# Performance work log

Measured on AMD Instinct MI355X. Metric: run time of the kernel, lower is better.

The kernel has to match this reference:

```python
import jax, jax.numpy as jnp
import numpy as np

HEAD = 16

def setup_inputs() -> dict:
    key = jax.random.key(0)
    ks = jax.random.split(key, 8)
    N, L, CT, C, H, W = 32, 77, 512, 512, 32, 32
    return {
        "feature": jax.random.normal(ks[0], (N, C, H, W), dtype=jnp.float32),
        "token": jax.random.normal(ks[1], (N, L, CT), dtype=jnp.float32),
        "Wv": jax.random.normal(ks[2], (C, CT), dtype=jnp.float32) * 0.02,
        "bv": jax.random.normal(ks[3], (C,), dtype=jnp.float32) * 0.02,
        "Wk": jax.random.normal(ks[4], (C, CT), dtype=jnp.float32) * 0.02,
        "bk": jax.random.normal(ks[5], (C,), dtype=jnp.float32) * 0.02,
        "Wq": jax.random.normal(ks[6], (CT, C), dtype=jnp.float32) * 0.02,
        "bq": jax.random.normal(ks[7], (CT,), dtype=jnp.float32) * 0.02,
    }

def reference(feature, token, Wv, bv, Wk, bk, Wq, bq):
    h = HEAD
    N, L, CT = token.shape
    # Faithful to torch: .view(N, CT, L) is a reshape, NOT a transpose
    tok = token.reshape(N, CT, L)
    # 1x1 conv1d projections: (N, C, L)
    v = jnp.einsum('oc,ncl->nol', Wv, tok) + bv[None, :, None]
    k = jnp.einsum('oc,ncl->nol', Wk, tok) + bk[None, :, None]
    v = v.reshape(N, h, -1, L)  # (N, h, d, L)
    k = k.reshape(N, h, -1, L)  # (N, h, d, L)
    # 1x1 conv2d query projection: C -> CT channels
    q = jnp.einsum('oc,nchw->nohw', Wq, feature) + bq[None, :, None, None]
    _, Cq, H, W = q.shape
    q = q.reshape(N, h, Cq // h, H * W).transpose(0, 1, 3, 2)  # (N, h, HW, d)
    scale = 1.0 / jnp.sqrt(jnp.float32(Cq / h))
    scores = jnp.einsum('nhqd,nhdl->nhql', q, k) * scale  # (N, h, HW, L)
    coef = jax.nn.softmax(scores, axis=3)
    proj = jnp.einsum('nhdl,nhql->nhdq', v, coef)  # (N, h, d, HW)
    out = feature + proj.reshape(N, -1, H, W)
    return (out, token)
```

## Files before the change

kernel.cpp:

```cpp
#include <hip/hip_runtime.h>
#include <hip/hip_bf16.h>

#define N_   32
#define L_   77
#define CT_  512
#define C_   512
#define HW_  1024
#define HEAD_ 16
#define DH_  32
#define NL_  (N_ * L_)
#define NLP_ 2496

typedef __attribute__((ext_vector_type(8))) short bf16x8;
typedef __attribute__((ext_vector_type(4))) short bf16x4;
typedef __attribute__((ext_vector_type(4))) float f32x4;

static __device__ __forceinline__ unsigned short f2bf(float f) {
    unsigned int u = __float_as_uint(f);
    unsigned int r = (u + 0x7fffu + ((u >> 16) & 1u)) >> 16;
    return (unsigned short)r;
}

__global__ __launch_bounds__(256) void prep_kernel(
    const float* __restrict__ token,
    const float* __restrict__ Wk, const float* __restrict__ bk,
    const float* __restrict__ Wv, const float* __restrict__ bv,
    unsigned short* __restrict__ tokT, unsigned short* __restrict__ Wkv,
    float* __restrict__ bkv)
{
    const int blk = blockIdx.x;
    const int t = threadIdx.x;
    if (blk < 256) {
        __shared__ float tile[64][81];
        const int n = blk >> 3, c0 = (blk & 7) * 64;
        const float* src = token + (size_t)n * (CT_ * L_) + (size_t)c0 * L_;
        for (int idx = t; idx < 64 * L_; idx += 256) {
            int cc = idx / L_, l = idx - cc * L_;
            tile[cc][l] = src[idx];
        }
        __syncthreads();
        for (int idx = t; idx < L_ * 16; idx += 256) {
            int l = idx >> 4, cq = (idx & 15) * 4;
            ushort4 h;
            h.x = f2bf(tile[cq + 0][l]);
            h.y = f2bf(tile[cq + 1][l]);
            h.z = f2bf(tile[cq + 2][l]);
            h.w = f2bf(tile[cq + 3][l]);
            *(ushort4*)&tokT[((size_t)(n * L_ + l)) * 512 + c0 + cq] = h;
        }
    } else {
        const int wb = blk - 256;
        const int m0 = wb * 32;
        for (int idx = t; idx < 32 * 128; idx += 256) {
            int mr = idx >> 7, c4 = (idx & 127) * 4;
            int m = m0 + mr;
            const float* src = (m < 512) ? (Wk + (size_t)m * 512 + c4)
                                         : (Wv + (size_t)(m - 512) * 512 + c4);
            float4 f = *(const float4*)src;
            ushort4 h; h.x = f2bf(f.x); h.y = f2bf(f.y); h.z = f2bf(f.z); h.w = f2bf(f.w);
            *(ushort4*)&Wkv[(size_t)m * 512 + c4] = h;
        }
        if (wb == 0) {
            for (int idx = t; idx < 1024; idx += 256)
                bkv[idx] = (idx < 512) ? bk[idx] : bv[idx - 512];
        }
    }
}

__global__ __launch_bounds__(256) void wconv_kernel(
    const float* __restrict__ Wq, unsigned short* __restrict__ Wqbf)
{
    const int m0 = blockIdx.x * 32;
    const int t = threadIdx.x;
    for (int idx = t; idx < 32 * 128; idx += 256) {
        int mr = idx >> 7, c4 = (idx & 127) * 4;
        float4 f = *(const float4*)&Wq[(size_t)(m0 + mr) * 512 + c4];
        ushort4 h; h.x = f2bf(f.x); h.y = f2bf(f.y); h.z = f2bf(f.z); h.w = f2bf(f.w);
        *(ushort4*)&Wqbf[(size_t)(m0 + mr) * 512 + c4] = h;
    }
}

__global__ __launch_bounds__(256) void kvgemm_kernel(
    const unsigned short* __restrict__ tokT,
    const unsigned short* __restrict__ Wkv,
    const float* __restrict__ bkv,
    float* __restrict__ kvbuf)
{
    __shared__ unsigned char Ab[128 * 128];
    __shared__ unsigned char Bb[64 * 128];

    const int blk = blockIdx.x;
    const int mt = blk / 39, nt = blk % 39;
    const int m0 = mt * 128, nl0 = nt * 64;
    const int t = threadIdx.x;
    const int lane = t & 63, w = t >> 6;
    const int wr = w >> 1, wc = w & 1;

    f32x4 acc[4][2];
#pragma unroll
    for (int i = 0; i < 4; ++i)
#pragma unroll
        for (int j = 0; j < 2; ++j) acc[i][j] = (f32x4){0.f, 0.f, 0.f, 0.f};

    for (int c0 = 0; c0 < 512; c0 += 64) {
        __syncthreads();
#pragma unroll
        for (int s = 0; s < 4; ++s) {
            int idx = t + s * 256;
            int row = idx >> 3, k8 = idx & 7;
            bf16x8 v = *(const bf16x8*)&Wkv[(size_t)(m0 + row) * 512 + c0 + k8 * 8];
            *(bf16x8*)(Ab + row * 128 + ((k8 * 16) ^ ((row & 7) << 4))) = v;
        }
#pragma unroll
        for (int s = 0; s < 2; ++s) {
            int idx = t + s * 256;
            int row = idx >> 3, k8 = idx & 7;
            bf16x8 v = *(const bf16x8*)&tokT[(size_t)(nl0 + row) * 512 + c0 + k8 * 8];
            *(bf16x8*)(Bb + row * 128 + ((k8 * 16) ^ ((row & 7) << 4))) = v;
        }
        __syncthreads();

#pragma unroll
        for (int ks = 0; ks < 2; ++ks) {
            const int kb = ks * 64 + (lane >> 4) * 16;
            bf16x8 a[4], b[2];
#pragma unroll
            for (int i = 0; i < 4; ++i) {
                int row = wr * 64 + i * 16 + (lane & 15);
                a[i] = *(const bf16x8*)(Ab + row * 128 + (kb ^ ((row & 7) << 4)));
            }
#pragma unroll
            for (int j = 0; j < 2; ++j) {
                int row = wc * 32 + j * 16 + (lane & 15);
                b[j] = *(const bf16x8*)(Bb + row * 128 + (kb ^ ((row & 7) << 4)));
            }
#pragma unroll
            for (int i = 0; i < 4; ++i)
#pragma unroll
                for (int j = 0; j < 2; ++j)
                    acc[i][j] = __builtin_amdgcn_mfma_f32_16x16x32_bf16(
                        a[i], b[j], acc[i][j], 0, 0, 0);
        }
    }

#pragma unroll
    for (int i = 0; i < 4; ++i) {
        int m = m0 + wr * 64 + i * 16 + (lane >> 4) * 4;
        float4 bias = *(const float4*)&bkv[m];
#pragma unroll
        for (int j = 0; j < 2; ++j) {
            int nl = nl0 + wc * 32 + j * 16 + (lane & 15);
            float4 o;
            o.x = acc[i][j][0] + bias.x;
            o.y = acc[i][j][1] + bias.y;
            o.z = acc[i][j][2] + bias.z;
            o.w = acc[i][j][3] + bias.w;
            *(float4*)&kvbuf[(size_t)nl * 1024 + m] = o;
        }
    }
}

__global__ __launch_bounds__(512) void qmfma_kernel(
    const float* __restrict__ feature,
    const unsigned short* __restrict__ Wqbf, const float* __restrict__ bq,
    unsigned short* __restrict__ qbuf)
{
    __shared__ unsigned char Ab[128 * 128];
    __shared__ unsigned char Bb[128 * 128];

    const int blk = blockIdx.x;
    const int pt = blk & 7;
    const int ot = (blk >> 3) & 3;
    const int n  = blk >> 5;
    const int o0 = ot * 128, p0 = pt * 128;
    const int t = threadIdx.x;
    const int lane = t & 63, w = t >> 6;
    const int wr = w >> 2, wc = w & 3;
    const int q15 = lane & 15, g = lane >> 4;

    f32x4 acc[4][2];
#pragma unroll
    for (int i = 0; i < 4; ++i)
#pragma unroll
        for (int j = 0; j < 2; ++j) acc[i][j] = (f32x4){0.f, 0.f, 0.f, 0.f};

    const float* featn = feature + (size_t)n * C_ * HW_;

    for (int c0 = 0; c0 < C_; c0 += 64) {
        __syncthreads();
#pragma unroll
        for (int s = 0; s < 2; ++s) {
            int idx = t + s * 512;
            int row = idx >> 3;
            int k8  = idx & 7;
            bf16x8 v = *(const bf16x8*)&Wqbf[(size_t)(o0 + row) * 512 + c0 + k8 * 8];
            *(bf16x8*)(Ab + row * 128 + ((k8 * 16) ^ ((row & 7) << 4))) = v;
        }
        {
            int p  = t & 127;
            int q2 = t >> 7;
#pragma unroll
            for (int it = 0; it < 4; ++it) {
                int cl = q2 * 16 + it * 4;
                const float* src = featn + (size_t)(c0 + cl) * HW_ + p0 + p;
                float f0 = src[0];
                float f1 = src[HW_];
                float f2 = src[2 * HW_];
                float f3 = src[3 * HW_];
                ushort4 h; h.x = f2bf(f0); h.y = f2bf(f1); h.z = f2bf(f2); h.w = f2bf(f3);
                *(ushort4*)(Bb + p * 128 + ((cl * 2) ^ ((p & 7) << 4))) = h;
            }
        }
        __syncthreads();

#pragma unroll
        for (int ks = 0; ks < 2; ++ks) {
            const int kb = ks * 64 + g * 16;
            bf16x8 a[4], b[2];
#pragma unroll
            for (int i = 0; i < 4; ++i) {
                int row = wr * 64 + i * 16 + q15;
                a[i] = *(const bf16x8*)(Ab + row * 128 + (kb ^ ((row & 7) << 4)));
            }
#pragma unroll
            for (int j = 0; j < 2; ++j) {
                int prow = wc * 32 + j * 16 + q15;
                b[j] = *(const bf16x8*)(Bb + prow * 128 + (kb ^ ((prow & 7) << 4)));
            }
#pragma unroll
            for (int i = 0; i < 4; ++i)
#pragma unroll
                for (int j = 0; j < 2; ++j)
                    acc[i][j] = __builtin_amdgcn_mfma_f32_16x16x32_bf16(
                        a[i], b[j], acc[i][j], 0, 0, 0);
        }
    }

    const float scale = 0.17677669529663687f;
#pragma unroll
    for (int i = 0; i < 4; ++i) {
#pragma unroll
        for (int r = 0; r < 4; ++r) {
            int o = o0 + wr * 64 + i * 16 + (lane >> 4) * 4 + r;
            float bias = bq[o];
#pragma unroll
            for (int j = 0; j < 2; ++j) {
                int p = p0 + wc * 32 + j * 16 + q15;
                qbuf[((size_t)n * C_ + o) * HW_ + p] = f2bf((acc[i][j][r] + bias) * scale);
            }
        }
    }
}

__global__ __launch_bounds__(256) void attn_kernel(
    const float* __restrict__ feature,
    const float* __restrict__ kvbuf,
    const unsigned short* __restrict__ qbuf,
    float* __restrict__ out)
{
    __shared__ unsigned char kl[80 * 64];
    __shared__ unsigned char vt[32 * 176];
    __shared__ unsigned char qs[256 * 64];

    const int blk = blockIdx.x;
    const int pc = blk & 3;
    const int h  = (blk >> 2) & 15;
    const int n  = blk >> 6;
    const int t = threadIdx.x;
    const int lane = t & 63, w = t >> 6;
    const int q15 = lane & 15, g = lane >> 4;
    const int pb = pc * 256;
    const int p0 = pb + w * 64;

    {
        const unsigned short* qsrc =
            qbuf + ((size_t)n * C_ + h * DH_) * HW_ + pb;
#pragma unroll
        for (int it = 0; it < 4; ++it) {
            int idx = t + it * 256;
            int oo = idx >> 5;
            int p8 = (idx & 31) * 8;
            bf16x8 v = *(const bf16x8*)(qsrc + (size_t)oo * HW_ + p8);
            int key = ((p8 >> 3) & 3) << 4;
            int slot = (((oo >> 3) << 4) ^ key) + (oo & 7) * 2;
            union { bf16x8 v8; unsigned short us[8]; } u; u.v8 = v;
#pragma unroll
            for (int j = 0; j < 8; ++j)
                *(unsigned short*)(qs + (p8 + j) * 64 + slot) = u.us[j];
        }
    }

    if (t < 48) *(unsigned int*)(kl + 77 * 64 + t * 4) = 0;
    if (t >= 96 && t < 96 + 352) {
        int u = t - 96;
        int d = u / 11, l = 77 + u % 11;
        *(unsigned short*)(vt + d * 176 + l * 2) = 0;
    }

    const float* kvb = kvbuf + (size_t)(n * L_) * 1024 + h * DH_;
    for (int idx = t; idx < L_ * 8; idx += 256) {
        int l = idx >> 3, dq = idx & 7;
        float4 k4 = *(const float4*)&kvb[(size_t)l * 1024 + dq * 4];
        ushort4 hk; hk.x = f2bf(k4.x); hk.y = f2bf(k4.y); hk.z = f2bf(k4.z); hk.w = f2bf(k4.w);
        int cx = dq >> 1, sub = (dq & 1) * 8;
        *(ushort4*)(kl + l * 64 + (((cx ^ (l & 3)) << 4) + sub)) = hk;
        float4 v4 = *(const float4*)&kvb[(size_t)l * 1024 + 512 + dq * 4];
        *(unsigned short*)(vt + (dq * 4 + 0) * 176 + l * 2) = f2bf(v4.x);
        *(unsigned short*)(vt + (dq * 4 + 1) * 176 + l * 2) = f2bf(v4.y);
        *(unsigned short*)(vt + (dq * 4 + 2) * 176 + l * 2) = f2bf(v4.z);
        *(unsigned short*)(vt + (dq * 4 + 3) * 176 + l * 2) = f2bf(v4.w);
    }
    __syncthreads();

    bf16x8 qf[4];
#pragma unroll
    for (int i = 0; i < 4; ++i) {
        int p = w * 64 + i * 16 + q15;
        qf[i] = *(const bf16x8*)(qs + p * 64 + ((g ^ ((p >> 3) & 3)) << 4));
    }
    bf16x8 kf[5];
#pragma unroll
    for (int lt = 0; lt < 5; ++lt) {
        int l = lt * 16 + q15;
        kf[lt] = *(const bf16x8*)(kl + l * 64 + ((g ^ (l & 3)) << 4));
    }
    bf16x4 vf[5][2];
#pragma unroll
    for (int lt = 0; lt < 5; ++lt)
#pragma unroll
        for (int dt = 0; dt < 2; ++dt)
            vf[lt][dt] = *(const bf16x4*)(vt + (dt * 16 + q15) * 176 + lt * 32 + g * 8);

    const float* featn = feature + ((size_t)n * C_ + h * DH_) * HW_;
    float* outn = out + ((size_t)n * C_ + h * DH_) * HW_;

#pragma unroll
    for (int i = 0; i < 4; ++i) {
        f32x4 s[5];
#pragma unroll
        for (int lt = 0; lt < 5; ++lt)
            s[lt] = __builtin_amdgcn_mfma_f32_16x16x32_bf16(
                kf[lt], qf[i], (f32x4){0.f, 0.f, 0.f, 0.f}, 0, 0, 0);

#pragma unroll
        for (int r = 0; r < 4; ++r)
            if (4 * g + r >= 13) s[4][r] = -3.0e38f;

        float mx = s[0][0];
#pragma unroll
        for (int lt = 0; lt < 5; ++lt)
#pragma unroll
            for (int r = 0; r < 4; ++r) mx = fmaxf(mx, s[lt][r]);
        mx = fmaxf(mx, __shfl_xor(mx, 16));
        mx = fmaxf(mx, __shfl_xor(mx, 32));

        float Z = 0.f;
#pragma unroll
        for (int lt = 0; lt < 5; ++lt)
#pragma unroll
            for (int r = 0; r < 4; ++r) {
                float e = __expf(s[lt][r] - mx);
                s[lt][r] = e;
                Z += e;
            }
        Z += __shfl_xor(Z, 16);
        Z += __shfl_xor(Z, 32);
        const float inv = 1.f / Z;

        unsigned int pk[5][2];
#pragma unroll
        for (int lt = 0; lt < 5; ++lt) {
            pk[lt][0] = (unsigned int)f2bf(s[lt][0] * inv)
                      | ((unsigned int)f2bf(s[lt][1] * inv) << 16);
            pk[lt][1] = (unsigned int)f2bf(s[lt][2] * inv)
                      | ((unsigned int)f2bf(s[lt][3] * inv) << 16);
        }

        f32x4 pv[2];
        pv[0] = (f32x4){0.f, 0.f, 0.f, 0.f};
        pv[1] = (f32x4){0.f, 0.f, 0.f, 0.f};
#pragma unroll
        for (int lt = 0; lt < 5; ++lt) {
            union { unsigned int u[2]; bf16x4 v; } pa;
            pa.u[0] = pk[lt][0];
            pa.u[1] = pk[lt][1];
#pragma unroll
            for (int dt = 0; dt < 2; ++dt)
                pv[dt] = __builtin_amdgcn_mfma_f32_16x16x16bf16_1k(
                    pa.v, vf[lt][dt], pv[dt], 0, 0, 0);
        }

#pragma unroll
        for (int dt = 0; dt < 2; ++dt) {
            size_t off = (size_t)(dt * 16 + q15) * HW_ + p0 + i * 16 + g * 4;
            float4 f = *(const float4*)&featn[off];
            float4 o;
            o.x = f.x + pv[dt][0];
            o.y = f.y + pv[dt][1];
            o.z = f.z + pv[dt][2];
            o.w = f.w + pv[dt][3];
            *(float4*)&outn[off] = o;
        }
    }
}

extern "C" void kernel_launch(void* const* d_in, const int* in_sizes, int n_in,
                              void* d_out, int out_size, void* d_ws, size_t ws_size,
                              hipStream_t stream)
{
    const float* feature = (const float*)d_in[0];
    const float* token   = (const float*)d_in[1];
    const float* Wv      = (const float*)d_in[2];
    const float* bv      = (const float*)d_in[3];
    const float* Wk      = (const float*)d_in[4];
    const float* bk      = (const float*)d_in[5];
    const float* Wq      = (const float*)d_in[6];
    const float* bq      = (const float*)d_in[7];
    float* out = (float*)d_out;

    float* kvbuf = (float*)d_ws;
    unsigned short* tokT = (unsigned short*)(kvbuf + (size_t)NLP_ * 1024);
    unsigned short* Wkv  = tokT + (size_t)NLP_ * 512;
    float* bkv = (float*)(Wkv + (size_t)1024 * 512);
    unsigned short* qbuf = (unsigned short*)(bkv + 1024);
    unsigned short* Wqbf = qbuf + (size_t)N_ * C_ * HW_;

    prep_kernel<<<288, 256, 0, stream>>>(token, Wk, bk, Wv, bv, tokT, Wkv, bkv);
    wconv_kernel<<<16, 256, 0, stream>>>(Wq, Wqbf);
    kvgemm_kernel<<<312, 256, 0, stream>>>(tokT, Wkv, bkv, kvbuf);
    qmfma_kernel<<<N_ * 32, 512, 0, stream>>>(feature, Wqbf, bq, qbuf);
    attn_kernel<<<N_ * HEAD_ * 4, 256, 0, stream>>>(feature, kvbuf, qbuf, out);

    hipMemcpyAsync(out + (size_t)N_ * C_ * HW_, token,
                   (size_t)N_ * L_ * CT_ * sizeof(float),
                   hipMemcpyDeviceToDevice, stream);
}
```

Measured before the change: 105.3 us.

## Restructure Q projection: stage full feature tile once, stream weights from global

The Q projection GEMM now has each block own all 512 output channels for a 64-pixel tile. The full 512-channel feature slice is converted to bf16 and staged in 64KB of shared memory once, so each feature element is read from global memory once instead of four times. Each wave reads its 64 weight rows directly from global or L2 instead of through shared memory, and the K-loop no longer has per-iteration barriers. The cost is 64KB of LDS per block, which lowers occupancy, and unstaged weight loads that rely on the cache hierarchy.

```diff
diff --git a/kernel.cpp b/kernel.cpp
--- a/kernel.cpp
+++ b/kernel.cpp
@@ -165,72 +165,61 @@
     const unsigned short* __restrict__ Wqbf, const float* __restrict__ bq,
     unsigned short* __restrict__ qbuf)
 {
-    __shared__ unsigned char Ab[128 * 128];
-    __shared__ unsigned char Bb[128 * 128];
+    __shared__ unsigned char Bb[64 * 1024];
 
     const int blk = blockIdx.x;
-    const int pt = blk & 7;
-    const int ot = (blk >> 3) & 3;
-    const int n  = blk >> 5;
-    const int o0 = ot * 128, p0 = pt * 128;
+    const int pt = blk & 15;
+    const int n  = blk >> 4;
+    const int p0 = pt * 64;
     const int t = threadIdx.x;
     const int lane = t & 63, w = t >> 6;
-    const int wr = w >> 2, wc = w & 3;
     const int q15 = lane & 15, g = lane >> 4;
 
-    f32x4 acc[4][2];
+    {
+        const float* featn = feature + (size_t)n * C_ * HW_ + p0;
+        int p  = t & 63;
+        int cq = (t >> 6) * 64;
+#pragma unroll
+        for (int it = 0; it < 16; ++it) {
+            int cl = cq + it * 4;
+            const float* src = featn + (size_t)cl * HW_ + p;
+            float f0 = src[0];
+            float f1 = src[HW_];
+            float f2 = src[2 * HW_];
+            float f3 = src[3 * HW_];
+            ushort4 h; h.x = f2bf(f0); h.y = f2bf(f1); h.z = f2bf(f2); h.w = f2bf(f3);
+            *(ushort4*)(Bb + p * 1024 + ((cl * 2) ^ ((p & 63) << 4))) = h;
+        }
+    }
+    __syncthreads();
+
+    f32x4 acc[4][4];
 #pragma unroll
     for (int i = 0; i < 4; ++i)
 #pragma unroll
-        for (int j = 0; j < 2; ++j) acc[i][j] = (f32x4){0.f, 0.f, 0.f, 0.f};
-
-    const float* featn = feature + (size_t)n * C_ * HW_;
-
-    for (int c0 = 0; c0 < C_; c0 += 64) {
-        __syncthreads();
-#pragma unroll
-        for (int s = 0; s < 2; ++s) {
-            int idx = t + s * 512;
-            int row = idx >> 3;
-            int k8  = idx & 7;
-            bf16x8 v = *(const bf16x8*)&Wqbf[(size_t)(o0 + row) * 512 + c0 + k8 * 8];
-            *(bf16x8*)(Ab + row * 128 + ((k8 * 16) ^ ((row & 7) << 4))) = v;
-        }
-        {
-            int p  = t & 127;
-            int q2 = t >> 7;
-#pragma unroll
-            for (int it = 0; it < 4; ++it) {
-                int cl = q2 * 16 + it * 4;
-                const float* src = featn + (size_t)(c0 + cl) * HW_ + p0 + p;
-                float f0 = src[0];
-                float f1 = src[HW_];
-                float f2 = src[2 * HW_];
-                float f3 = src[3 * HW_];
-                ushort4 h; h.x = f2bf(f0); h.y = f2bf(f1); h.z = f2bf(f2); h.w = f2bf(f3);
-                *(ushort4*)(Bb + p * 128 + ((cl * 2) ^ ((p & 7) << 4))) = h;
-            }
-        }
-        __syncthreads();
-
+        for (int j = 0; j < 4; ++j) acc[i][j] = (f32x4){0.f, 0.f, 0.f, 0.f};
+
+    const unsigned short* wbase = Wqbf + (size_t)(w * 64) * 512;
+
+    for (int c0 = 0; c0 < 512; c0 += 64) {
 #pragma unroll
         for (int ks = 0; ks < 2; ++ks) {
-            const int kb = ks * 64 + g * 16;
-            bf16x8 a[4], b[2];
+            const int cb = c0 * 2 + ks * 64 + g * 16;
+            bf16x8 a[4], b[4];
 #pragma unroll
             for (int i = 0; i < 4; ++i) {
-                int row = wr * 64 + i * 16 + q15;
-                a[i] = *(const bf16x8*)(Ab + row * 128 + (kb ^ ((row & 7) << 4)));
-            }
-#pragma unroll
-            for (int j = 0; j < 2; ++j) {
-                int prow = wc * 32 + j * 16 + q15;
-                b[j] = *(const bf16x8*)(Bb + prow * 128 + (kb ^ ((prow & 7) << 4)));
+                int row = i * 16 + q15;
+                a[i] = *(const bf16x8*)&wbase[(size_t)row * 512 + c0 + ks * 32 + g * 8];
+            }
+#pragma unroll
+            for (int j = 0; j < 4; ++j) {
+                int prow = j * 16 + q15;
+                b[j] = *(const bf16x8*)(Bb + prow * 1024 + (cb ^ ((prow & 63) << 4)));
             }
 #pragma unroll
             for (int i = 0; i < 4; ++i)
 #pragma unroll
-                for (int j = 0; j < 2; ++j)
+                for (int j = 0; j < 4; ++j)
                     acc[i][j] = __builtin_amdgcn_mfma_f32_16x16x32_bf16(
                         a[i], b[j], acc[i][j], 0, 0, 0);
         }
@@ -241,11 +230,11 @@
     for (int i = 0; i < 4; ++i) {
 #pragma unroll
         for (int r = 0; r < 4; ++r) {
-            int o = o0 + wr * 64 + i * 16 + (lane >> 4) * 4 + r;
+            int o = w * 64 + i * 16 + (lane >> 4) * 4 + r;
             float bias = bq[o];
 #pragma unroll
-            for (int j = 0; j < 2; ++j) {
-                int p = p0 + wc * 32 + j * 16 + q15;
+            for (int j = 0; j < 4; ++j) {
+                int p = p0 + j * 16 + q15;
                 qbuf[((size_t)n * C_ + o) * HW_ + p] = f2bf((acc[i][j][r] + bias) * scale);
             }
         }
@@ -428,7 +417,7 @@
     prep_kernel<<<288, 256, 0, stream>>>(token, Wk, bk, Wv, bv, tokT, Wkv, bkv);
     wconv_kernel<<<16, 256, 0, stream>>>(Wq, Wqbf);
     kvgemm_kernel<<<312, 256, 0, stream>>>(tokT, Wkv, bkv, kvbuf);
-    qmfma_kernel<<<N_ * 32, 512, 0, stream>>>(feature, Wqbf, bq, qbuf);
+    qmfma_kernel<<<N_ * 16, 512, 0, stream>>>(feature, Wqbf, bq, qbuf);
     attn_kernel<<<N_ * HEAD_ * 4, 256, 0, stream>>>(feature, kvbuf, qbuf, out);
 
     hipMemcpyAsync(out + (size_t)N_ * C_ * HW_, token,
```

Result: slower. 113.0 us (+7.3%).
